# Optimization experiments

Hardware: AMD Instinct MI355X
Metric: run time of the kernel (lower is better)

## Reference

```python
import jax, jax.numpy as jnp
import numpy as np

ALPHA = 0.2          # LeakyReLU negative slope (Alpha)
NEG_INF = -9e15      # mask value used by pygat-style GAT


def _masked_attention(Wh, a_src, a_dst, mask):
    """Wh: [H,N,d], a_src/a_dst: [H,d], mask: [N,N] (nonzero = edge).
    Returns attention-aggregated features [H,N,d]."""
    f_src = jnp.einsum('hnd,hd->hn', Wh, a_src)   # [H,N]
    f_dst = jnp.einsum('hnd,hd->hn', Wh, a_dst)   # [H,N]
    e = jax.nn.leaky_relu(f_src[:, :, None] + f_dst[:, None, :], ALPHA)  # [H,N,N]
    e = jnp.where(mask[None, :, :] > 0, e, NEG_INF)
    att = jax.nn.softmax(e, axis=-1)              # masked softmax over neighbors
    return jnp.einsum('hnm,hmd->hnd', att, Wh)    # [H,N,d]


def setup_inputs() -> dict:
    key = jax.random.key(0)
    ks = jax.random.split(key, 8)
    N, F_in, D, H = 4096, 512, 64, 8
    x = jax.random.normal(ks[0], (N, F_in), dtype=jnp.float32)
    adj = jax.random.randint(ks[1], (N, N), 0, 2, dtype=jnp.int32)
    s = 0.1
    W = jax.random.normal(ks[2], (H, F_in, D), dtype=jnp.float32) * s
    a_src = jax.random.normal(ks[3], (H, D), dtype=jnp.float32) * s
    a_dst = jax.random.normal(ks[4], (H, D), dtype=jnp.float32) * s
    W_o = jax.random.normal(ks[5], (H * D, D), dtype=jnp.float32) * s
    ao_src = jax.random.normal(ks[6], (D,), dtype=jnp.float32) * s
    ao_dst = jax.random.normal(ks[7], (D,), dtype=jnp.float32) * s
    return {"x": x, "adj": adj, "W": W, "a_src": a_src, "a_dst": a_dst,
            "W_o": W_o, "ao_src": ao_src, "ao_dst": ao_dst}


def reference(x, adj, W, a_src, a_dst, W_o, ao_src, ao_dst):
    N = x.shape[0]
    # --- multi-head layer (concat=True: ELU per head, concat on feature dim) ---
    Wh = jnp.einsum('nf,hfd->hnd', x, W)                     # [H,N,d]
    h1 = jax.nn.elu(_masked_attention(Wh, a_src, a_dst, adj))  # [H,N,d]
    h_cat = jnp.transpose(h1, (1, 0, 2)).reshape(N, -1)      # [N, H*d]
    # --- output head (concat=False: no ELU inside layer) ---
    Who = (h_cat @ W_o)[None]                                # [1,N,d]
    h2 = _masked_attention(Who, ao_src[None], ao_dst[None], adj)[0]  # [N,d]
    # GAT.forward: activation (ELU) then log_softmax over dim=1
    return jax.nn.log_softmax(jax.nn.elu(h2), axis=1)
```

## Files before the change

### kernel.cpp

```cpp
#include <hip/hip_runtime.h>
#include <hip/hip_bf16.h>
#include <math.h>

#define N_NODES 4096
#define FDIM 512
#define D 64
#define H 8
#define NWORDS (N_NODES / 64)

typedef __attribute__((ext_vector_type(8))) short bf16x8;
typedef __attribute__((ext_vector_type(4))) float f32x4;

__device__ inline short f2bf(float x) {
    return (short)((__builtin_bit_cast(unsigned int, x) + 0x8000u) >> 16);
}

__device__ inline int sext_bit(unsigned int v, int j) {
#if defined(__has_builtin) && __has_builtin(__builtin_amdgcn_sbfe)
    return __builtin_amdgcn_sbfe((int)v, j, 1);
#else
    return ((int)(v << (31 - j))) >> 31;
#endif
}

__device__ inline void gl2lds16(const void* g, void* l) {
#if defined(__has_builtin) && __has_builtin(__builtin_amdgcn_global_load_lds)
    __builtin_amdgcn_global_load_lds(
        (const __attribute__((address_space(1))) unsigned int*)g,
        (__attribute__((address_space(3))) unsigned int*)l, 16, 0, 0);
#else
    *(uint4*)l = *(const uint4*)g;
#endif
}

__global__ void k_bits(const int* __restrict__ adj, unsigned long long* __restrict__ bits) {
    int idx = blockIdx.x * 256 + threadIdx.x;
    unsigned long long m = __ballot(adj[idx] != 0);
    if ((threadIdx.x & 63) == 0) bits[idx >> 6] = m;
}

__global__ void k_wfrag(const float* __restrict__ Wsrc, short* __restrict__ WF) {
    const size_t idx = (size_t)blockIdx.x * 256 + threadIdx.x;
    const int d = idx & 63;
    const int k = (int)(idx >> 6) & 511;
    const int h = (int)(idx >> 15);
    WF[(((size_t)h * 64 + (k >> 3)) * 64 + d) * 8 + (k & 7)] = f2bf(Wsrc[idx]);
}

__global__ void __launch_bounds__(256) k_gemm(
    const float* __restrict__ X, const short* __restrict__ WF,
    const float* __restrict__ av, const float* __restrict__ bv,
    float* __restrict__ Out, short* __restrict__ WBout,
    float* __restrict__ fs, float* __restrict__ fd) {
    const int h  = blockIdx.y;
    const int i0 = blockIdx.x * 64;
    const int t = threadIdx.x, w = t >> 6, lane = t & 63;
    const int li = lane & 15, quad = lane >> 4, k0 = quad * 8;
    const int row_a = i0 + w * 16 + li;
    const float* __restrict__ Xr  = X + (size_t)row_a * FDIM;
    const short* __restrict__ WFh = WF + (size_t)h * 64 * D * 8;

    f32x4 c0 = {0.f, 0.f, 0.f, 0.f}, c1 = c0, c2 = c0, c3 = c0;
    #pragma unroll 4
    for (int kt = 0; kt < FDIM; kt += 32) {
        float4 x0 = *(const float4*)&Xr[kt + k0];
        float4 x1 = *(const float4*)&Xr[kt + k0 + 4];
        bf16x8 a;
        a[0] = f2bf(x0.x); a[1] = f2bf(x0.y); a[2] = f2bf(x0.z); a[3] = f2bf(x0.w);
        a[4] = f2bf(x1.x); a[5] = f2bf(x1.y); a[6] = f2bf(x1.z); a[7] = f2bf(x1.w);
        const short* bb = WFh + (size_t)((kt >> 3) + quad) * (D * 8) + li * 8;
        bf16x8 b0 = *(const bf16x8*)(bb);
        bf16x8 b1 = *(const bf16x8*)(bb + 128);
        bf16x8 b2 = *(const bf16x8*)(bb + 256);
        bf16x8 b3 = *(const bf16x8*)(bb + 384);
        c0 = __builtin_amdgcn_mfma_f32_16x16x32_bf16(a, b0, c0, 0, 0, 0);
        c1 = __builtin_amdgcn_mfma_f32_16x16x32_bf16(a, b1, c1, 0, 0, 0);
        c2 = __builtin_amdgcn_mfma_f32_16x16x32_bf16(a, b2, c2, 0, 0, 0);
        c3 = __builtin_amdgcn_mfma_f32_16x16x32_bf16(a, b3, c3, 0, 0, 0);
    }
    float av4[4], bv4[4];
    #pragma unroll
    for (int t4 = 0; t4 < 4; ++t4) {
        av4[t4] = av[h * D + t4 * 16 + li];
        bv4[t4] = bv[h * D + t4 * 16 + li];
    }
    float tiles[4][4];
    #pragma unroll
    for (int r = 0; r < 4; ++r) { tiles[0][r] = c0[r]; tiles[1][r] = c1[r]; tiles[2][r] = c2[r]; tiles[3][r] = c3[r]; }
    #pragma unroll
    for (int r = 0; r < 4; ++r) {
        const int row = i0 + w * 16 + quad * 4 + r;
        float pa = 0.f, pb = 0.f;
        #pragma unroll
        for (int t4 = 0; t4 < 4; ++t4) {
            const float v = tiles[t4][r];
            const int d = t4 * 16 + li;
            Out[((size_t)h * N_NODES + row) * D + d] = v;
            WBout[((size_t)h * (N_NODES / 8) + (row >> 3)) * (D * 8) + d * 8 + (row & 7)] = f2bf(v);
            pa += v * av4[t4];
            pb += v * bv4[t4];
        }
        #pragma unroll
        for (int off = 1; off < 16; off <<= 1) {
            pa += __shfl_xor(pa, off);
            pb += __shfl_xor(pb, off);
        }
        if (li == 0) {
            fs[(size_t)h * N_NODES + row] = pa;
            fd[(size_t)h * N_NODES + row] = pb;
        }
    }
}

__global__ void k_stats(const float* __restrict__ fd, const float* __restrict__ Wh,
                        float* __restrict__ gmax, float* __restrict__ colmean) {
    const int h = blockIdx.y;
    const int t = threadIdx.x;
    __shared__ float cs[4][64];
    if (blockIdx.x == 16) {
        float m = -INFINITY;
        for (int i = t; i < N_NODES; i += 256) m = fmaxf(m, fd[(size_t)h * N_NODES + i]);
        #pragma unroll
        for (int off = 32; off > 0; off >>= 1) m = fmaxf(m, __shfl_xor(m, off));
        if ((t & 63) == 0) cs[t >> 6][0] = m;
        __syncthreads();
        if (t == 0)
            gmax[h] = fmaxf(fmaxf(cs[0][0], cs[1][0]), fmaxf(cs[2][0], cs[3][0]));
        return;
    }
    const int i0 = blockIdx.x * 256;
    const int d  = t & 63, rg = t >> 6;
    const float* __restrict__ base = Wh + (size_t)h * N_NODES * D;
    float s = 0.f;
    #pragma unroll 8
    for (int r = rg; r < 256; r += 4) s += base[(size_t)(i0 + r) * D + d];
    cs[rg][d] = s;
    __syncthreads();
    if (t < 64)
        atomicAdd(&colmean[h * D + t],
                  (cs[0][t] + cs[1][t] + cs[2][t] + cs[3][t]) * (1.f / (float)N_NODES));
}

__global__ void k_prep(const float* __restrict__ fs, const float* __restrict__ fd,
                       const float* __restrict__ gmax,
                       float* __restrict__ Rout, float* __restrict__ Ed,
                       float* __restrict__ Eg) {
    const int h = blockIdx.y;
    const size_t o = (size_t)h * N_NODES + blockIdx.x * 256 + threadIdx.x;
    const float fsv = fs[o], fdv = fd[o], gm = gmax[h];
    Rout[o] = __expf(-0.8f * (fsv + gm));
    Ed[o]   = __expf(fdv - gm);
    Eg[o]   = __expf(0.2f * (fdv - gm));
}

__global__ void __launch_bounds__(256) k_accum(
    const unsigned int* __restrict__ bits32,
    const short* __restrict__ WB,
    const float* __restrict__ Rb, const float* __restrict__ Edb,
    const float* __restrict__ Egb,
    float* __restrict__ num, float* __restrict__ den, int kslab) {

    __shared__ __align__(16) short Bt[2][16 * 64 * 8];
    __shared__ __align__(16) float EG[2][256];

    const int h = blockIdx.y, i0 = blockIdx.x * 64, slab = blockIdx.z;
    const int t = threadIdx.x, w = t >> 6, lane = t & 63;
    const int li = lane & 15, quad = lane >> 4, k0 = quad * 8;
    const int    i_row = i0 + w * 16 + li;
    const size_t ho    = (size_t)h * N_NODES;
    const float  Rv    = Rb[ho + i_row];
    const float* __restrict__ Ed = Edb + ho;
    const float* __restrict__ Eg = Egb + ho;
    const short* __restrict__ Bh = WB + (size_t)h * (N_NODES / 8) * D * 8;
    const unsigned int* __restrict__ brow = bits32 + (size_t)i_row * (NWORDS * 2);

    f32x4 c0 = {0.f, 0.f, 0.f, 0.f}, c1 = c0, c2 = c0, c3 = c0, c5 = c0;
    bf16x8 ones;
    #pragma unroll
    for (int j = 0; j < 8; ++j) ones[j] = (short)0x3F80;

    const int k_beg = slab * kslab;
    const int ntile = kslab / 128;

    auto stage = [&](int buf, int jt) {
        const short* src = Bh + (size_t)(jt >> 3) * (D * 8);
        #pragma unroll
        for (int p = 0; p < 4; ++p)
            gl2lds16(src + (size_t)(p * 256 + t) * 8, &Bt[buf][(p * 256 + t) * 8]);
        if (w == 0) {
            const float* egsrc = (lane < 32) ? &Ed[jt + lane * 4]
                                             : &Eg[jt + (lane - 32) * 4];
            gl2lds16(egsrc, &EG[buf][lane * 4]);
        }
    };

    stage(0, k_beg);
    uint4 bwv = *(const uint4*)&brow[k_beg >> 5];
    for (int tile = 0; tile < ntile; ++tile) {
        const int jt = k_beg + tile * 128;
        __syncthreads();
        if (tile + 1 < ntile) stage((tile + 1) & 1, jt + 128);
        const short* Bl  = Bt[tile & 1];
        const float* EGl = EG[tile & 1];
        const unsigned int bwa[4] = {bwv.x, bwv.y, bwv.z, bwv.w};
        if (tile + 1 < ntile) bwv = *(const uint4*)&brow[(jt + 128) >> 5];
        #pragma unroll
        for (int s = 0; s < 4; ++s) {
            const float4 e0 = *(const float4*)&EGl[s * 32 + k0];
            const float4 e1 = *(const float4*)&EGl[s * 32 + k0 + 4];
            const float4 g0 = *(const float4*)&EGl[128 + s * 32 + k0];
            const float4 g1 = *(const float4*)&EGl[128 + s * 32 + k0 + 4];
            const unsigned int byt = (bwa[s] >> k0) & 0xFFu;
            float ev[8], gv[8];
            ev[0] = e0.x; ev[1] = e0.y; ev[2] = e0.z; ev[3] = e0.w;
            ev[4] = e1.x; ev[5] = e1.y; ev[6] = e1.z; ev[7] = e1.w;
            gv[0] = g0.x; gv[1] = g0.y; gv[2] = g0.z; gv[3] = g0.w;
            gv[4] = g1.x; gv[5] = g1.y; gv[6] = g1.z; gv[7] = g1.w;
            unsigned int pa[8];
            #pragma unroll
            for (int j = 0; j < 8; ++j) {
                const float p = fmaxf(ev[j], gv[j] * Rv);
                pa[j] = __builtin_bit_cast(unsigned int, p)
                        & (unsigned int)sext_bit(byt, j);
            }
            bf16x8 a;
            unsigned int* au = (unsigned int*)&a;
            au[0] = __builtin_amdgcn_perm(pa[1], pa[0], 0x07060302);
            au[1] = __builtin_amdgcn_perm(pa[3], pa[2], 0x07060302);
            au[2] = __builtin_amdgcn_perm(pa[5], pa[4], 0x07060302);
            au[3] = __builtin_amdgcn_perm(pa[7], pa[6], 0x07060302);

            const short* bb = Bl + (size_t)((s * 4 + quad) * 64 + li) * 8;
            bf16x8 b0 = *(const bf16x8*)(bb);
            bf16x8 b1 = *(const bf16x8*)(bb + 128);
            bf16x8 b2 = *(const bf16x8*)(bb + 256);
            bf16x8 b3 = *(const bf16x8*)(bb + 384);
            c0 = __builtin_amdgcn_mfma_f32_16x16x32_bf16(a, b0, c0, 0, 0, 0);
            c1 = __builtin_amdgcn_mfma_f32_16x16x32_bf16(a, b1, c1, 0, 0, 0);
            c2 = __builtin_amdgcn_mfma_f32_16x16x32_bf16(a, b2, c2, 0, 0, 0);
            c3 = __builtin_amdgcn_mfma_f32_16x16x32_bf16(a, b3, c3, 0, 0, 0);
            c5 = __builtin_amdgcn_mfma_f32_16x16x32_bf16(a, ones, c5, 0, 0, 0);
        }
    }

    const size_t so = (size_t)(slab * gridDim.y + h);
    float tiles[4][4];
    #pragma unroll
    for (int r = 0; r < 4; ++r) { tiles[0][r] = c0[r]; tiles[1][r] = c1[r]; tiles[2][r] = c2[r]; tiles[3][r] = c3[r]; }
    #pragma unroll
    for (int t4 = 0; t4 < 4; ++t4)
        #pragma unroll
        for (int r = 0; r < 4; ++r) {
            const int row = i0 + w * 16 + quad * 4 + r;
            num[(so * N_NODES + row) * D + t4 * 16 + li] = tiles[t4][r];
        }
    if (li == 0)
        #pragma unroll
        for (int r = 0; r < 4; ++r)
            den[so * N_NODES + i0 + w * 16 + quad * 4 + r] = c5[r];
}

__global__ void k_post1(const float* __restrict__ num, const float* __restrict__ den,
                        const float* __restrict__ colmean, float* __restrict__ hcat) {
    const int h   = blockIdx.y;
    const int i0  = blockIdx.x * 64;
    const int t   = threadIdx.x;
    const int row = i0 + (t >> 2);
    const int cb  = (t & 3) * 16;
    const size_t HN = (size_t)gridDim.y * N_NODES;
    const size_t r0 = (size_t)h * N_NODES + row;
    const float dsum = den[r0] + den[HN + r0];
    const bool  uni  = !(dsum > 0.f);
    const float linv = uni ? 0.f : 1.f / dsum;
    #pragma unroll
    for (int c = 0; c < 4; ++c) {
        const int col = cb + c * 4;
        float4 a = *(const float4*)&num[r0 * D + col];
        float4 b = *(const float4*)&num[(HN + r0) * D + col];
        float4 v;
        v.x = (a.x + b.x) * linv; v.y = (a.y + b.y) * linv;
        v.z = (a.z + b.z) * linv; v.w = (a.w + b.w) * linv;
        if (uni) v = *(const float4*)&colmean[h * D + col];
        v.x = v.x > 0.f ? v.x : __expf(v.x) - 1.f;
        v.y = v.y > 0.f ? v.y : __expf(v.y) - 1.f;
        v.z = v.z > 0.f ? v.z : __expf(v.z) - 1.f;
        v.w = v.w > 0.f ? v.w : __expf(v.w) - 1.f;
        *(float4*)&hcat[(size_t)row * (H * D) + h * D + col] = v;
    }
}

__global__ void k_lsm(const float* __restrict__ num, const float* __restrict__ den,
                      const float* __restrict__ cm, float* __restrict__ out) {
    const int n    = blockIdx.x * 4 + (threadIdx.x >> 6);
    const int lane = threadIdx.x & 63;
    float v = 0.f, ds = 0.f;
    #pragma unroll
    for (int s = 0; s < 8; ++s) v  += num[((size_t)s * N_NODES + n) * D + lane];
    #pragma unroll
    for (int s = 0; s < 8; ++s) ds += den[(size_t)s * N_NODES + n];
    v = (ds > 0.f) ? v / ds : cm[lane];
    v = v > 0.f ? v : __expf(v) - 1.f;
    float mx = v;
    #pragma unroll
    for (int off = 32; off > 0; off >>= 1) mx = fmaxf(mx, __shfl_xor(mx, off));
    float ex = __expf(v - mx);
    float sum = ex;
    #pragma unroll
    for (int off = 32; off > 0; off >>= 1) sum += __shfl_xor(sum, off);
    out[(size_t)n * D + lane] = (v - mx) - __logf(sum);
}

extern "C" void kernel_launch(void* const* d_in, const int* in_sizes, int n_in,
                              void* d_out, int out_size, void* d_ws, size_t ws_size,
                              hipStream_t stream) {
    const float* x      = (const float*)d_in[0];
    const int*   adj    = (const int*)d_in[1];
    const float* W      = (const float*)d_in[2];
    const float* a_src  = (const float*)d_in[3];
    const float* a_dst  = (const float*)d_in[4];
    const float* W_o    = (const float*)d_in[5];
    const float* ao_src = (const float*)d_in[6];
    const float* ao_dst = (const float*)d_in[7];
    float* out = (float*)d_out;

    char* wsp = (char*)d_ws;
    size_t off = 0;
    auto alloc = [&](size_t bytes) -> void* {
        void* p = wsp + off;
        off += (bytes + 255) & ~(size_t)255;
        return p;
    };
    unsigned long long* adj_bits = (unsigned long long*)alloc((size_t)N_NODES * NWORDS * 8);
    short* WF1   = (short*)alloc((size_t)H * 64 * D * 8 * 2);
    short* WoF   = (short*)alloc((size_t)64 * D * 8 * 2);
    float* Wh    = (float*)alloc((size_t)H * N_NODES * D * 4);
    short* WhB   = (short*)alloc((size_t)H * N_NODES * D * 2);
    float* fs1   = (float*)alloc((size_t)H * N_NODES * 4);
    float* fd1   = (float*)alloc((size_t)H * N_NODES * 4);
    float* gmax1 = (float*)alloc((size_t)H * 4);
    float* cm1   = (float*)alloc((size_t)H * D * 4);
    float* R1    = (float*)alloc((size_t)H * N_NODES * 4);
    float* Ed1   = (float*)alloc((size_t)H * N_NODES * 4);
    float* Ee1   = (float*)alloc((size_t)H * N_NODES * 4);
    float* num1  = (float*)alloc((size_t)2 * H * N_NODES * D * 4);
    float* den1  = (float*)alloc((size_t)2 * H * N_NODES * 4);
    float* hcat  = (float*)alloc((size_t)N_NODES * H * D * 4);
    float* Who   = (float*)alloc((size_t)N_NODES * D * 4);
    short* WhoB  = (short*)alloc((size_t)N_NODES * D * 2);
    float* fs2   = (float*)alloc((size_t)N_NODES * 4);
    float* fd2   = (float*)alloc((size_t)N_NODES * 4);
    float* gmax2 = (float*)alloc(4);
    float* cm2   = (float*)alloc((size_t)D * 4);
    float* R2    = (float*)alloc((size_t)N_NODES * 4);
    float* Ed2   = (float*)alloc((size_t)N_NODES * 4);
    float* Ee2   = (float*)alloc((size_t)N_NODES * 4);
    float* num2  = (float*)alloc((size_t)8 * N_NODES * D * 4);
    float* den2  = (float*)alloc((size_t)8 * N_NODES * 4);

    const unsigned int* bits32 = (const unsigned int*)adj_bits;

    hipMemsetAsync(cm1, 0, (size_t)H * D * 4, stream);
    hipMemsetAsync(cm2, 0, (size_t)D * 4, stream);

    k_bits <<<dim3(N_NODES * N_NODES / 256), dim3(256), 0, stream>>>(adj, adj_bits);
    k_wfrag<<<dim3(H * FDIM * D / 256), dim3(256), 0, stream>>>(W, WF1);
    k_wfrag<<<dim3(FDIM * D / 256), dim3(256), 0, stream>>>(W_o, WoF);

    k_gemm <<<dim3(N_NODES / 64, H), dim3(256), 0, stream>>>(x, WF1, a_src, a_dst,
                                                             Wh, WhB, fs1, fd1);
    k_stats<<<dim3(17, H), dim3(256), 0, stream>>>(fd1, Wh, gmax1, cm1);
    k_prep <<<dim3(N_NODES / 256, H), dim3(256), 0, stream>>>(fs1, fd1, gmax1, R1, Ed1, Ee1);
    k_accum<<<dim3(N_NODES / 64, H, 2), dim3(256), 0, stream>>>(bits32, WhB, R1, Ed1, Ee1,
                                                                num1, den1, N_NODES / 2);
    k_post1<<<dim3(N_NODES / 64, H), dim3(256), 0, stream>>>(num1, den1, cm1, hcat);

    k_gemm <<<dim3(N_NODES / 64, 1), dim3(256), 0, stream>>>(hcat, WoF, ao_src, ao_dst,
                                                             Who, WhoB, fs2, fd2);
    k_stats<<<dim3(17, 1), dim3(256), 0, stream>>>(fd2, Who, gmax2, cm2);
    k_prep <<<dim3(N_NODES / 256, 1), dim3(256), 0, stream>>>(fs2, fd2, gmax2, R2, Ed2, Ee2);
    k_accum<<<dim3(N_NODES / 64, 1, 8), dim3(256), 0, stream>>>(bits32, WhoB, R2, Ed2, Ee2,
                                                                num2, den2, N_NODES / 8);
    k_lsm  <<<dim3(N_NODES / 4), dim3(256), 0, stream>>>(num2, den2, cm2, out);
}
```

Baseline: 227.2 us.

## Process two 16-row fragments per wave in k_accum to reuse B tiles

Each wave in k_accum now computes two 16-row MFMA fragments (128 rows per block) instead of one. The B fragments and E/G values loaded from LDS are reused across both row groups, halving LDS and global staging traffic per output row. To keep the grid occupied, the second layer splits K into 16 slabs instead of 8, which doubles the partial-sum buffers that k_lsm must reduce. The cost is more registers per wave, which may lower occupancy.

Result: no change. 230.7 us (+1.6%).

```diff
diff --git a/kernel.cpp b/kernel.cpp
--- a/kernel.cpp
+++ b/kernel.cpp
@@ -163,18 +163,26 @@
     __shared__ __align__(16) short Bt[2][16 * 64 * 8];
     __shared__ __align__(16) float EG[2][256];
 
-    const int h = blockIdx.y, i0 = blockIdx.x * 64, slab = blockIdx.z;
+    const int h = blockIdx.y, i0 = blockIdx.x * 128, slab = blockIdx.z;
     const int t = threadIdx.x, w = t >> 6, lane = t & 63;
     const int li = lane & 15, quad = lane >> 4, k0 = quad * 8;
-    const int    i_row = i0 + w * 16 + li;
-    const size_t ho    = (size_t)h * N_NODES;
-    const float  Rv    = Rb[ho + i_row];
+    const int    r0 = i0 + w * 32 + li;
+    const int    r1 = r0 + 16;
+    const size_t ho = (size_t)h * N_NODES;
+    const float  Rv0 = Rb[ho + r0], Rv1 = Rb[ho + r1];
     const float* __restrict__ Ed = Edb + ho;
     const float* __restrict__ Eg = Egb + ho;
     const short* __restrict__ Bh = WB + (size_t)h * (N_NODES / 8) * D * 8;
-    const unsigned int* __restrict__ brow = bits32 + (size_t)i_row * (NWORDS * 2);
-
-    f32x4 c0 = {0.f, 0.f, 0.f, 0.f}, c1 = c0, c2 = c0, c3 = c0, c5 = c0;
+    const unsigned int* __restrict__ brow0 = bits32 + (size_t)r0 * (NWORDS * 2);
+    const unsigned int* __restrict__ brow1 = bits32 + (size_t)r1 * (NWORDS * 2);
+
+    f32x4 acc[2][4], c5[2];
+    #pragma unroll
+    for (int f = 0; f < 2; ++f) {
+        #pragma unroll
+        for (int q = 0; q < 4; ++q) acc[f][q] = (f32x4){0.f, 0.f, 0.f, 0.f};
+        c5[f] = (f32x4){0.f, 0.f, 0.f, 0.f};
+    }
     bf16x8 ones;
     #pragma unroll
     for (int j = 0; j < 8; ++j) ones[j] = (short)0x3F80;
@@ -195,69 +203,88 @@
     };
 
     stage(0, k_beg);
-    uint4 bwv = *(const uint4*)&brow[k_beg >> 5];
+    uint4 bw0 = *(const uint4*)&brow0[k_beg >> 5];
+    uint4 bw1 = *(const uint4*)&brow1[k_beg >> 5];
     for (int tile = 0; tile < ntile; ++tile) {
         const int jt = k_beg + tile * 128;
         __syncthreads();
         if (tile + 1 < ntile) stage((tile + 1) & 1, jt + 128);
         const short* Bl  = Bt[tile & 1];
         const float* EGl = EG[tile & 1];
-        const unsigned int bwa[4] = {bwv.x, bwv.y, bwv.z, bwv.w};
-        if (tile + 1 < ntile) bwv = *(const uint4*)&brow[(jt + 128) >> 5];
+        const unsigned int bwa0[4] = {bw0.x, bw0.y, bw0.z, bw0.w};
+        const unsigned int bwa1[4] = {bw1.x, bw1.y, bw1.z, bw1.w};
+        if (tile + 1 < ntile) {
+            bw0 = *(const uint4*)&brow0[(jt + 128) >> 5];
+            bw1 = *(const uint4*)&brow1[(jt + 128) >> 5];
+        }
         #pragma unroll
         for (int s = 0; s < 4; ++s) {
             const float4 e0 = *(const float4*)&EGl[s * 32 + k0];
             const float4 e1 = *(const float4*)&EGl[s * 32 + k0 + 4];
             const float4 g0 = *(const float4*)&EGl[128 + s * 32 + k0];
             const float4 g1 = *(const float4*)&EGl[128 + s * 32 + k0 + 4];
-            const unsigned int byt = (bwa[s] >> k0) & 0xFFu;
+            const unsigned int byt0 = (bwa0[s] >> k0) & 0xFFu;
+            const unsigned int byt1 = (bwa1[s] >> k0) & 0xFFu;
             float ev[8], gv[8];
             ev[0] = e0.x; ev[1] = e0.y; ev[2] = e0.z; ev[3] = e0.w;
             ev[4] = e1.x; ev[5] = e1.y; ev[6] = e1.z; ev[7] = e1.w;
             gv[0] = g0.x; gv[1] = g0.y; gv[2] = g0.z; gv[3] = g0.w;
             gv[4] = g1.x; gv[5] = g1.y; gv[6] = g1.z; gv[7] = g1.w;
-            unsigned int pa[8];
+            unsigned int pa0[8], pa1[8];
             #pragma unroll
             for (int j = 0; j < 8; ++j) {
-                const float p = fmaxf(ev[j], gv[j] * Rv);
-                pa[j] = __builtin_bit_cast(unsigned int, p)
-                        & (unsigned int)sext_bit(byt, j);
+                const float p0 = fmaxf(ev[j], gv[j] * Rv0);
+                const float p1 = fmaxf(ev[j], gv[j] * Rv1);
+                pa0[j] = __builtin_bit_cast(unsigned int, p0)
+                         & (unsigned int)sext_bit(byt0, j);
+                pa1[j] = __builtin_bit_cast(unsigned int, p1)
+                         & (unsigned int)sext_bit(byt1, j);
             }
-            bf16x8 a;
-            unsigned int* au = (unsigned int*)&a;
-            au[0] = __builtin_amdgcn_perm(pa[1], pa[0], 0x07060302);
-            au[1] = __builtin_amdgcn_perm(pa[3], pa[2], 0x07060302);
-            au[2] = __builtin_amdgcn_perm(pa[5], pa[4], 0x07060302);
-            au[3] = __builtin_amdgcn_perm(pa[7], pa[6], 0x07060302);
+            bf16x8 a0, a1;
+            unsigned int* au0 = (unsigned int*)&a0;
+            unsigned int* au1 = (unsigned int*)&a1;
+            au0[0] = __builtin_amdgcn_perm(pa0[1], pa0[0], 0x07060302);
+            au0[1] = __builtin_amdgcn_perm(pa0[3], pa0[2], 0x07060302);
+            au0[2] = __builtin_amdgcn_perm(pa0[5], pa0[4], 0x07060302);
+            au0[3] = __builtin_amdgcn_perm(pa0[7], pa0[6], 0x07060302);
+            au1[0] = __builtin_amdgcn_perm(pa1[1], pa1[0], 0x07060302);
+            au1[1] = __builtin_amdgcn_perm(pa1[3], pa1[2], 0x07060302);
+            au1[2] = __builtin_amdgcn_perm(pa1[5], pa1[4], 0x07060302);
+            au1[3] = __builtin_amdgcn_perm(pa1[7], pa1[6], 0x07060302);
 
             const short* bb = Bl + (size_t)((s * 4 + quad) * 64 + li) * 8;
             bf16x8 b0 = *(const bf16x8*)(bb);
             bf16x8 b1 = *(const bf16x8*)(bb + 128);
             bf16x8 b2 = *(const bf16x8*)(bb + 256);
             bf16x8 b3 = *(const bf16x8*)(bb + 384);
-            c0 = __builtin_amdgcn_mfma_f32_16x16x32_bf16(a, b0, c0, 0, 0, 0);
-            c1 = __builtin_amdgcn_mfma_f32_16x16x32_bf16(a, b1, c1, 0, 0, 0);
-            c2 = __builtin_amdgcn_mfma_f32_16x16x32_bf16(a, b2, c2, 0, 0, 0);
-            c3 = __builtin_amdgcn_mfma_f32_16x16x32_bf16(a, b3, c3, 0, 0, 0);
-            c5 = __builtin_amdgcn_mfma_f32_16x16x32_bf16(a, ones, c5, 0, 0, 0);
+            acc[0][0] = __builtin_amdgcn_mfma_f32_16x16x32_bf16(a0, b0, acc[0][0], 0, 0, 0);
+            acc[0][1] = __builtin_amdgcn_mfma_f32_16x16x32_bf16(a0, b1, acc[0][1], 0, 0, 0);
+            acc[0][2] = __builtin_amdgcn_mfma_f32_16x16x32_bf16(a0, b2, acc[0][2], 0, 0, 0);
+            acc[0][3] = __builtin_amdgcn_mfma_f32_16x16x32_bf16(a0, b3, acc[0][3], 0, 0, 0);
+            c5[0]     = __builtin_amdgcn_mfma_f32_16x16x32_bf16(a0, ones, c5[0], 0, 0, 0);
+            acc[1][0] = __builtin_amdgcn_mfma_f32_16x16x32_bf16(a1, b0, acc[1][0], 0, 0, 0);
+            acc[1][1] = __builtin_amdgcn_mfma_f32_16x16x32_bf16(a1, b1, acc[1][1], 0, 0, 0);
+            acc[1][2] = __builtin_amdgcn_mfma_f32_16x16x32_bf16(a1, b2, acc[1][2], 0, 0, 0);
+            acc[1][3] = __builtin_amdgcn_mfma_f32_16x16x32_bf16(a1, b3, acc[1][3], 0, 0, 0);
+            c5[1]     = __builtin_amdgcn_mfma_f32_16x16x32_bf16(a1, ones, c5[1], 0, 0, 0);
         }
     }
 
     const size_t so = (size_t)(slab * gridDim.y + h);
-    float tiles[4][4];
-    #pragma unroll
-    for (int r = 0; r < 4; ++r) { tiles[0][r] = c0[r]; tiles[1][r] = c1[r]; tiles[2][r] = c2[r]; tiles[3][r] = c3[r]; }
-    #pragma unroll
-    for (int t4 = 0; t4 < 4; ++t4)
-        #pragma unroll
-        for (int r = 0; r < 4; ++r) {
-            const int row = i0 + w * 16 + quad * 4 + r;
-            num[(so * N_NODES + row) * D + t4 * 16 + li] = tiles[t4][r];
-        }
-    if (li == 0)
-        #pragma unroll
-        for (int r = 0; r < 4; ++r)
-            den[so * N_NODES + i0 + w * 16 + quad * 4 + r] = c5[r];
+    #pragma unroll
+    for (int f = 0; f < 2; ++f) {
+        #pragma unroll
+        for (int t4 = 0; t4 < 4; ++t4)
+            #pragma unroll
+            for (int r = 0; r < 4; ++r) {
+                const int row = i0 + w * 32 + f * 16 + quad * 4 + r;
+                num[(so * N_NODES + row) * D + t4 * 16 + li] = acc[f][t4][r];
+            }
+        if (li == 0)
+            #pragma unroll
+            for (int r = 0; r < 4; ++r)
+                den[so * N_NODES + i0 + w * 32 + f * 16 + quad * 4 + r] = c5[f][r];
+    }
 }
 
 __global__ void k_post1(const float* __restrict__ num, const float* __restrict__ den,
@@ -295,9 +322,9 @@
     const int lane = threadIdx.x & 63;
     float v = 0.f, ds = 0.f;
     #pragma unroll
-    for (int s = 0; s < 8; ++s) v  += num[((size_t)s * N_NODES + n) * D + lane];
-    #pragma unroll
-    for (int s = 0; s < 8; ++s) ds += den[(size_t)s * N_NODES + n];
+    for (int s = 0; s < 16; ++s) v  += num[((size_t)s * N_NODES + n) * D + lane];
+    #pragma unroll
+    for (int s = 0; s < 16; ++s) ds += den[(size_t)s * N_NODES + n];
     v = (ds > 0.f) ? v / ds : cm[lane];
     v = v > 0.f ? v : __expf(v) - 1.f;
     float mx = v;
@@ -354,8 +381,8 @@
     float* R2    = (float*)alloc((size_t)N_NODES * 4);
     float* Ed2   = (float*)alloc((size_t)N_NODES * 4);
     float* Ee2   = (float*)alloc((size_t)N_NODES * 4);
-    float* num2  = (float*)alloc((size_t)8 * N_NODES * D * 4);
-    float* den2  = (float*)alloc((size_t)8 * N_NODES * 4);
+    float* num2  = (float*)alloc((size_t)16 * N_NODES * D * 4);
+    float* den2  = (float*)alloc((size_t)16 * N_NODES * 4);
 
     const unsigned int* bits32 = (const unsigned int*)adj_bits;
 
@@ -370,15 +397,15 @@
                                                              Wh, WhB, fs1, fd1);
     k_stats<<<dim3(17, H), dim3(256), 0, stream>>>(fd1, Wh, gmax1, cm1);
     k_prep <<<dim3(N_NODES / 256, H), dim3(256), 0, stream>>>(fs1, fd1, gmax1, R1, Ed1, Ee1);
-    k_accum<<<dim3(N_NODES / 64, H, 2), dim3(256), 0, stream>>>(bits32, WhB, R1, Ed1, Ee1,
-                                                                num1, den1, N_NODES / 2);
+    k_accum<<<dim3(N_NODES / 128, H, 2), dim3(256), 0, stream>>>(bits32, WhB, R1, Ed1, Ee1,
+                                                                 num1, den1, N_NODES / 2);
     k_post1<<<dim3(N_NODES / 64, H), dim3(256), 0, stream>>>(num1, den1, cm1, hcat);
 
     k_gemm <<<dim3(N_NODES / 64, 1), dim3(256), 0, stream>>>(hcat, WoF, ao_src, ao_dst,
                                                              Who, WhoB, fs2, fd2);
     k_stats<<<dim3(17, 1), dim3(256), 0, stream>>>(fd2, Who, gmax2, cm2);
     k_prep <<<dim3(N_NODES / 256, 1), dim3(256), 0, stream>>>(fs2, fd2, gmax2, R2, Ed2, Ee2);
-    k_accum<<<dim3(N_NODES / 64, 1, 8), dim3(256), 0, stream>>>(bits32, WhoB, R2, Ed2, Ee2,
-                                                                num2, den2, N_NODES / 8);
+    k_accum<<<dim3(N_NODES / 128, 1, 16), dim3(256), 0, stream>>>(bits32, WhoB, R2, Ed2, Ee2,
+                                                                  num2, den2, N_NODES / 16);
     k_lsm  <<<dim3(N_NODES / 4), dim3(256), 0, stream>>>(num2, den2, cm2, out);
 }
```
